# Kernel tuning notes

Hardware: AMD Instinct MI355X
Metric: run time of the kernel (lower is better)

Reference implementation:

```python
import jax, jax.numpy as jnp
import numpy as np

LEAKY_SLOPE = 0.05        # self.alpha is overwritten to 0.05 in __init__
NEG_INF = -9.0e15         # masking constant from the source
THRESH = 0.5              # connection_threshold

B, N, F = 8, 2048, 128


def setup_inputs() -> dict:
    key = jax.random.key(0)
    k1, k2, k3, k4, k5 = jax.random.split(key, 5)
    h = jax.random.normal(k1, (B, N, F), dtype=jnp.float32)
    W = jax.random.normal(k2, (F, F), dtype=jnp.float32) * (1.414 / np.sqrt(F))
    a = jax.random.normal(k3, (2 * F, 1), dtype=jnp.float32) * 0.1
    A1 = jax.random.normal(k4, (4 * N, N), dtype=jnp.float32) * (1.414 / np.sqrt(N))
    A2 = jax.random.normal(k5, (N, 4 * N), dtype=jnp.float32) * (1.414 / np.sqrt(4 * N))
    return {"h": h, "W": W, "a": a, "A1": A1, "A2": A2}


def reference(h, W, a, A1, A2):
    f = W.shape[0]
    # Wh = h @ W^T  (torch Linear stores weight as [out, in])
    Wh = jnp.einsum('bnf,gf->bng', h, W)                       # [B,N,F]
    # additive GAT scores: e[b,i,j] = leaky_relu(Wh_i.a1 + Wh_j.a2)
    Wh1 = Wh @ a[:f, :]                                        # [B,N,1]
    Wh2 = Wh @ a[f:, :]                                        # [B,N,1]
    e = Wh1 + jnp.swapaxes(Wh2, 1, 2)                          # [B,N,N]
    e = jnp.where(e > 0, e, LEAKY_SLOPE * e)                   # LeakyReLU(0.05)
    # learned adjacency gate over last dim (computed in the original forward
    # but never used for the returned output -> dead code; kept for fidelity)
    hid = jax.nn.sigmoid(jnp.einsum('bij,hj->bih', e, A1))     # [B,N,4N]
    adj = jax.nn.sigmoid(e + jnp.einsum('bih,jh->bij', hid, A2))
    adj = jnp.where(adj > THRESH, adj, 0.0)                    # unused downstream
    # masked softmax attention over e itself
    attention = jax.nn.softmax(jnp.where(e > 0, e, NEG_INF), axis=2)
    # dropout is identity in eval mode (training=False)
    h_prime = jnp.einsum('bij,bjf->bif', attention, Wh)        # [B,N,F]
    return jax.nn.elu(h_prime)                                 # concat=True branch
```

## Files before the change

### kernel.cpp

```cpp
#include <hip/hip_runtime.h>
#include <math.h>

#define BB 8
#define NN 2048
#define FF 128
#define CH 128
#define CHSZ 16

__global__ __launch_bounds__(512) void k1_wh(
        const float* __restrict__ h, const float* __restrict__ W,
        const float* __restrict__ a, float* __restrict__ Wh,
        float* __restrict__ s1, float* __restrict__ s2) {
    __shared__ __align__(16) float Wt[64][132];
    __shared__ float hs[64][65];
    const int tid = threadIdx.x;
    const int row0 = blockIdx.x * 64;
    const int gq = tid & 15;
    const int rq = tid >> 4;

    float acc[2][8];
#pragma unroll
    for (int r = 0; r < 2; ++r)
#pragma unroll
        for (int g = 0; g < 8; ++g) acc[r][g] = 0.f;

    for (int half = 0; half < 2; ++half) {
        __syncthreads();
        for (int idx = tid; idx < 64 * 128; idx += 512) {
            int g = idx >> 6, fl = idx & 63;
            Wt[fl][g] = W[g * 128 + half * 64 + fl];
        }
        for (int idx = tid; idx < 64 * 64; idx += 512) {
            int r = idx >> 6, fl = idx & 63;
            hs[r][fl] = h[(row0 + r) * 128 + half * 64 + fl];
        }
        __syncthreads();
        for (int fl = 0; fl < 64; ++fl) {
            float4 w0 = *(const float4*)&Wt[fl][gq * 8];
            float4 w1 = *(const float4*)&Wt[fl][gq * 8 + 4];
            float h0 = hs[rq * 2 + 0][fl];
            float h1 = hs[rq * 2 + 1][fl];
            acc[0][0] += h0 * w0.x; acc[0][1] += h0 * w0.y;
            acc[0][2] += h0 * w0.z; acc[0][3] += h0 * w0.w;
            acc[0][4] += h0 * w1.x; acc[0][5] += h0 * w1.y;
            acc[0][6] += h0 * w1.z; acc[0][7] += h0 * w1.w;
            acc[1][0] += h1 * w0.x; acc[1][1] += h1 * w0.y;
            acc[1][2] += h1 * w0.z; acc[1][3] += h1 * w0.w;
            acc[1][4] += h1 * w1.x; acc[1][5] += h1 * w1.y;
            acc[1][6] += h1 * w1.z; acc[1][7] += h1 * w1.w;
        }
    }

    float a1v[8], a2v[8];
#pragma unroll
    for (int g = 0; g < 8; ++g) {
        a1v[g] = a[gq * 8 + g];
        a2v[g] = a[128 + gq * 8 + g];
    }
#pragma unroll
    for (int r = 0; r < 2; ++r) {
        int row = row0 + rq * 2 + r;
        *(float4*)&Wh[row * 128 + gq * 8] =
            make_float4(acc[r][0], acc[r][1], acc[r][2], acc[r][3]);
        *(float4*)&Wh[row * 128 + gq * 8 + 4] =
            make_float4(acc[r][4], acc[r][5], acc[r][6], acc[r][7]);
        float p1 = 0.f, p2 = 0.f;
#pragma unroll
        for (int g = 0; g < 8; ++g) {
            p1 += acc[r][g] * a1v[g];
            p2 += acc[r][g] * a2v[g];
        }
#pragma unroll
        for (int s = 1; s < 16; s <<= 1) {
            p1 += __shfl_xor(p1, s, 64);
            p2 += __shfl_xor(p2, s, 64);
        }
        if (gq == 0) { s1[row] = p1; s2[row] = p2; }
    }
}

__global__ __launch_bounds__(512) void k2_rank(
        const float* __restrict__ s2, const float* __restrict__ s1,
        int* __restrict__ idxs, float* __restrict__ ps,
        int* __restrict__ lo_arr) {
    __shared__ __align__(16) float ls[NN];
    __shared__ int part[8][64];
    __shared__ int lpart[8][64];
    __shared__ float wmax[8];
    const int t = threadIdx.x;
    const int blk = blockIdx.x;
    const int b = blk >> 5;
    const int seg = blk & 31;
    const int base = b * NN;
    float4* ls4 = (float4*)ls;
    const float4* g4 = (const float4*)(s2 + base);
    float m;
    {
        float4 v4 = g4[t];
        ls4[t] = v4;
        m = fmaxf(fmaxf(v4.x, v4.y), fmaxf(v4.z, v4.w));
    }
#pragma unroll
    for (int s = 1; s < 64; s <<= 1) m = fmaxf(m, __shfl_xor(m, s, 64));
    if ((t & 63) == 0) wmax[t >> 6] = m;
    __syncthreads();
    float M = wmax[0];
#pragma unroll
    for (int i = 1; i < 8; ++i) M = fmaxf(M, wmax[i]);
    const int jj = t & 63;
    const int w  = t >> 6;
    const int j  = seg * 64 + jj;
    const float v = ls[j];
    const float s1v = s1[base + j];
    int rank = 0, cnt = 0;
#pragma unroll 8
    for (int q = 0; q < 64; ++q) {
        float4 kv = ls4[w * 64 + q];
        int kg = w * 256 + q * 4;
        rank += (kv.x < v) | ((kv.x == v) & (kg + 0 < j));
        rank += (kv.y < v) | ((kv.y == v) & (kg + 1 < j));
        rank += (kv.z < v) | ((kv.z == v) & (kg + 2 < j));
        rank += (kv.w < v) | ((kv.w == v) & (kg + 3 < j));
        cnt += (s1v + kv.x <= 0.f);
        cnt += (s1v + kv.y <= 0.f);
        cnt += (s1v + kv.z <= 0.f);
        cnt += (s1v + kv.w <= 0.f);
    }
    part[w][jj] = rank;
    lpart[w][jj] = cnt;
    __syncthreads();
    if (t < 64) {
        int r = 0, lo = 0;
#pragma unroll
        for (int ww = 0; ww < 8; ++ww) {
            r  += part[ww][t];
            lo += lpart[ww][t];
        }
        int jg = seg * 64 + t;
        float vv = ls[jg];
        idxs[base + r] = jg;
        ps[base + r] = expf(vv - M);
        lo_arr[base + jg] = lo;
    }
}

__global__ __launch_bounds__(128) void k3_scan(
        const float* __restrict__ Wh, const int* __restrict__ idxs,
        const float* __restrict__ ps,
        float* __restrict__ partial, float* __restrict__ psuf,
        float* __restrict__ chunktot, float* __restrict__ chunku,
        float* __restrict__ chunkp) {
    const int blk = blockIdx.x;
    const int b = blk >> 7, c = blk & 127;
    const int base = b * NN;
    const int f = threadIdx.x;
    float acc = 0.f, accu = 0.f, pacc = 0.f;
#pragma unroll
    for (int tt = CHSZ - 1; tt >= 0; --tt) {
        int r = c * CHSZ + tt;
        int jj = idxs[base + r];
        float pv = ps[base + r];
        float w = Wh[(base + jj) * 128 + f];
        acc += pv * w;
        accu += w;
        pacc += pv;
        partial[(base + r) * 128 + f] = acc;
        if (f == 0) psuf[base + r] = pacc;
    }
    chunktot[(b * CH + c) * 128 + f] = acc;
    chunku[(b * CH + c) * 128 + f] = accu;
    if (f == 0) chunkp[b * CH + c] = pacc;
}

__global__ __launch_bounds__(512) void k4_merged(
        const float* __restrict__ chunktot, const float* __restrict__ chunku,
        const float* __restrict__ chunkp,
        const int* __restrict__ lo_arr, const float* __restrict__ psuf,
        const float* __restrict__ partial, float* __restrict__ out) {
    __shared__ __align__(16) float cs[CH][132];
    __shared__ __align__(16) float mvp[4][132];
    __shared__ __align__(16) float mv[128];
    __shared__ float lp[CH];
    const int tid = threadIdx.x;
    const int blk = blockIdx.x;
    const int b = blk >> 5;
    const int base = b * NN;

    {
        const int f  = tid & 127;
        const int r0 = tid >> 7;
        float su = 0.f;
#pragma unroll 4
        for (int i = 0; i < 32; ++i) {
            int c = r0 + i * 4;
            cs[c][f] = chunktot[(b * CH + c) * 128 + f];
            su += chunku[(b * CH + c) * 128 + f];
        }
        mvp[r0][f] = su;
        if (tid < CH) lp[tid] = chunkp[b * CH + tid];
    }
    __syncthreads();
    if (tid < 128)
        mv[tid] = (mvp[0][tid] + mvp[1][tid] + mvp[2][tid] + mvp[3][tid])
                  * (1.f / (float)NN);

    for (int s = 1; s < CH; s <<= 1) {
        float tmp[32];
#pragma unroll
        for (int i = 0; i < 32; ++i) {
            int c = (tid >> 7) + i * 4;
            int f = tid & 127;
            tmp[i] = (c + s < CH) ? cs[c + s][f] : 0.f;
        }
        float ap = 0.f;
        if (tid < CH && tid + s < CH) ap = lp[tid + s];
        __syncthreads();
#pragma unroll
        for (int i = 0; i < 32; ++i) {
            int c = (tid >> 7) + i * 4;
            int f = tid & 127;
            cs[c][f] += tmp[i];
        }
        if (tid < CH) lp[tid] += ap;
        __syncthreads();
    }

#pragma unroll
    for (int pass = 0; pass < 4; ++pass) {
        const int rowg = blk * 64 + pass * 16 + (tid >> 5);
        const int fq = (tid & 31) * 4;
        const int lo = lo_arr[rowg];
        float4 v;
        if (lo == NN) {
            v = make_float4(mv[fq], mv[fq + 1], mv[fq + 2], mv[fq + 3]);
        } else {
            const int c = lo >> 4;
            float4 pp = *(const float4*)&partial[(base + lo) * 128 + fq];
            float4 csv = make_float4(0.f, 0.f, 0.f, 0.f);
            float lps = 0.f;
            if (c < CH - 1) {
                csv = *(const float4*)&cs[c + 1][fq];
                lps = lp[c + 1];
            }
            float den = psuf[base + lo] + lps;
            v.x = (pp.x + csv.x) / den;
            v.y = (pp.y + csv.y) / den;
            v.z = (pp.z + csv.z) / den;
            v.w = (pp.w + csv.w) / den;
        }
        v.x = (v.x > 0.f) ? v.x : expm1f(v.x);
        v.y = (v.y > 0.f) ? v.y : expm1f(v.y);
        v.z = (v.z > 0.f) ? v.z : expm1f(v.z);
        v.w = (v.w > 0.f) ? v.w : expm1f(v.w);
        *(float4*)&out[rowg * 128 + fq] = v;
    }
}

extern "C" void kernel_launch(void* const* d_in, const int* in_sizes, int n_in,
                              void* d_out, int out_size, void* d_ws, size_t ws_size,
                              hipStream_t stream) {
    (void)in_sizes; (void)n_in; (void)out_size; (void)ws_size;
    const float* h = (const float*)d_in[0];
    const float* W = (const float*)d_in[1];
    const float* a = (const float*)d_in[2];
    float* out = (float*)d_out;

    float* Wh       = (float*)d_ws;
    float* partial  = Wh + 2097152;
    float* s1       = partial + 2097152;
    float* s2       = s1 + 16384;
    float* ps       = s2 + 16384;
    float* psuf     = ps + 16384;
    int*   idxs     = (int*)(psuf + 16384);
    int*   lo_arr   = idxs + 16384;
    float* chunktot = (float*)(lo_arr + 16384);
    float* chunku   = chunktot + 131072;
    float* chunkp   = chunku + 131072;

    k1_wh<<<BB * NN / 64, 512, 0, stream>>>(h, W, a, Wh, s1, s2);
    k2_rank<<<BB * 32, 512, 0, stream>>>(s2, s1, idxs, ps, lo_arr);
    k3_scan<<<BB * CH, 128, 0, stream>>>(Wh, idxs, ps, partial, psuf,
                                         chunktot, chunku, chunkp);
    k4_merged<<<BB * 32, 512, 0, stream>>>(chunktot, chunku, chunkp,
                                           lo_arr, psuf, partial, out);
}
```

Before: 188.2 us.

## Use split-bf16 MFMA for Wh projection and register-based suffix scan in k4

The Wh = h·W^T projection now runs on MFMA bf16 instructions, with each fp32 operand split into high and low bf16 parts. Three MFMAs per tile (hi·hi, hi·lo, lo·hi) approximate fp32 accuracy. The block drops to 256 threads and W is converted into LDS in both halves per block. Separately, k4 replaces its log-step shared-memory suffix scan over 128 chunks, which needed many syncthreads, with a per-thread serial suffix sum over 32 chunks plus a small cross-segment offset, and does a wavefront-shuffle scan for chunkp. The split-bf16 product drops the lo·lo term, so it risks small precision loss.

New measurement: 170.0 us. -9.6%, faster.

```diff
diff --git a/kernel.cpp b/kernel.cpp
--- a/kernel.cpp
+++ b/kernel.cpp
@@ -7,75 +7,110 @@
 #define CH 128
 #define CHSZ 16
 
-__global__ __launch_bounds__(512) void k1_wh(
+typedef __attribute__((ext_vector_type(8))) short short8;
+typedef __attribute__((ext_vector_type(4))) float f32x4;
+
+__device__ __forceinline__ ushort f2bf(float x) {
+    uint u = __float_as_uint(x);
+    uint r = (u + 0x7FFFu + ((u >> 16) & 1u)) >> 16;
+    return (ushort)r;
+}
+__device__ __forceinline__ float bf2f(ushort x) {
+    return __uint_as_float(((uint)x) << 16);
+}
+
+__global__ __launch_bounds__(256) void k1_wh(
         const float* __restrict__ h, const float* __restrict__ W,
         const float* __restrict__ a, float* __restrict__ Wh,
         float* __restrict__ s1, float* __restrict__ s2) {
-    __shared__ __align__(16) float Wt[64][132];
-    __shared__ float hs[64][65];
+    __shared__ __align__(16) ushort Whi[128][136];
+    __shared__ __align__(16) ushort Wlo[128][136];
+    __shared__ __align__(16) ushort hhi[64][136];
+    __shared__ __align__(16) ushort hlo[64][136];
     const int tid = threadIdx.x;
     const int row0 = blockIdx.x * 64;
-    const int gq = tid & 15;
-    const int rq = tid >> 4;
-
-    float acc[2][8];
-#pragma unroll
-    for (int r = 0; r < 2; ++r)
-#pragma unroll
-        for (int g = 0; g < 8; ++g) acc[r][g] = 0.f;
-
-    for (int half = 0; half < 2; ++half) {
-        __syncthreads();
-        for (int idx = tid; idx < 64 * 128; idx += 512) {
-            int g = idx >> 6, fl = idx & 63;
-            Wt[fl][g] = W[g * 128 + half * 64 + fl];
-        }
-        for (int idx = tid; idx < 64 * 64; idx += 512) {
-            int r = idx >> 6, fl = idx & 63;
-            hs[r][fl] = h[(row0 + r) * 128 + half * 64 + fl];
-        }
-        __syncthreads();
-        for (int fl = 0; fl < 64; ++fl) {
-            float4 w0 = *(const float4*)&Wt[fl][gq * 8];
-            float4 w1 = *(const float4*)&Wt[fl][gq * 8 + 4];
-            float h0 = hs[rq * 2 + 0][fl];
-            float h1 = hs[rq * 2 + 1][fl];
-            acc[0][0] += h0 * w0.x; acc[0][1] += h0 * w0.y;
-            acc[0][2] += h0 * w0.z; acc[0][3] += h0 * w0.w;
-            acc[0][4] += h0 * w1.x; acc[0][5] += h0 * w1.y;
-            acc[0][6] += h0 * w1.z; acc[0][7] += h0 * w1.w;
-            acc[1][0] += h1 * w0.x; acc[1][1] += h1 * w0.y;
-            acc[1][2] += h1 * w0.z; acc[1][3] += h1 * w0.w;
-            acc[1][4] += h1 * w1.x; acc[1][5] += h1 * w1.y;
-            acc[1][6] += h1 * w1.z; acc[1][7] += h1 * w1.w;
-        }
-    }
-
-    float a1v[8], a2v[8];
-#pragma unroll
-    for (int g = 0; g < 8; ++g) {
-        a1v[g] = a[gq * 8 + g];
-        a2v[g] = a[128 + gq * 8 + g];
-    }
-#pragma unroll
-    for (int r = 0; r < 2; ++r) {
-        int row = row0 + rq * 2 + r;
-        *(float4*)&Wh[row * 128 + gq * 8] =
-            make_float4(acc[r][0], acc[r][1], acc[r][2], acc[r][3]);
-        *(float4*)&Wh[row * 128 + gq * 8 + 4] =
-            make_float4(acc[r][4], acc[r][5], acc[r][6], acc[r][7]);
-        float p1 = 0.f, p2 = 0.f;
-#pragma unroll
-        for (int g = 0; g < 8; ++g) {
-            p1 += acc[r][g] * a1v[g];
-            p2 += acc[r][g] * a2v[g];
-        }
-#pragma unroll
-        for (int s = 1; s < 16; s <<= 1) {
-            p1 += __shfl_xor(p1, s, 64);
-            p2 += __shfl_xor(p2, s, 64);
-        }
-        if (gq == 0) { s1[row] = p1; s2[row] = p2; }
+
+    for (int i = tid; i < 4096; i += 256) {
+        int g = i >> 5, k4 = (i & 31) * 4;
+        float4 wv = *(const float4*)&W[g * 128 + k4];
+        ushort h0 = f2bf(wv.x), h1 = f2bf(wv.y), h2 = f2bf(wv.z), h3 = f2bf(wv.w);
+        ushort l0 = f2bf(wv.x - bf2f(h0)), l1 = f2bf(wv.y - bf2f(h1));
+        ushort l2 = f2bf(wv.z - bf2f(h2)), l3 = f2bf(wv.w - bf2f(h3));
+        uint2 hw, lw;
+        hw.x = (uint)h0 | ((uint)h1 << 16); hw.y = (uint)h2 | ((uint)h3 << 16);
+        lw.x = (uint)l0 | ((uint)l1 << 16); lw.y = (uint)l2 | ((uint)l3 << 16);
+        *(uint2*)&Whi[g][k4] = hw;
+        *(uint2*)&Wlo[g][k4] = lw;
+    }
+    for (int i = tid; i < 2048; i += 256) {
+        int r = i >> 5, k4 = (i & 31) * 4;
+        float4 hv = *(const float4*)&h[(row0 + r) * 128 + k4];
+        ushort h0 = f2bf(hv.x), h1 = f2bf(hv.y), h2 = f2bf(hv.z), h3 = f2bf(hv.w);
+        ushort l0 = f2bf(hv.x - bf2f(h0)), l1 = f2bf(hv.y - bf2f(h1));
+        ushort l2 = f2bf(hv.z - bf2f(h2)), l3 = f2bf(hv.w - bf2f(h3));
+        uint2 hw, lw;
+        hw.x = (uint)h0 | ((uint)h1 << 16); hw.y = (uint)h2 | ((uint)h3 << 16);
+        lw.x = (uint)l0 | ((uint)l1 << 16); lw.y = (uint)l2 | ((uint)l3 << 16);
+        *(uint2*)&hhi[r][k4] = hw;
+        *(uint2*)&hlo[r][k4] = lw;
+    }
+    __syncthreads();
+
+    const int lane = tid & 63;
+    const int wid = tid >> 6;
+    const int gl = lane & 15;
+    const int kg = lane >> 4;
+    const int lr = wid * 16 + gl;
+
+    f32x4 acc[8];
+#pragma unroll
+    for (int gt = 0; gt < 8; ++gt) acc[gt] = (f32x4){0.f, 0.f, 0.f, 0.f};
+
+#pragma unroll
+    for (int t = 0; t < 4; ++t) {
+        const int k0 = t * 32 + kg * 8;
+        short8 ah = *(const short8*)&hhi[lr][k0];
+        short8 al = *(const short8*)&hlo[lr][k0];
+#pragma unroll
+        for (int gt = 0; gt < 8; ++gt) {
+            const int g = gt * 16 + gl;
+            short8 bh = *(const short8*)&Whi[g][k0];
+            short8 bl = *(const short8*)&Wlo[g][k0];
+            acc[gt] = __builtin_amdgcn_mfma_f32_16x16x32_bf16(ah, bh, acc[gt], 0, 0, 0);
+            acc[gt] = __builtin_amdgcn_mfma_f32_16x16x32_bf16(ah, bl, acc[gt], 0, 0, 0);
+            acc[gt] = __builtin_amdgcn_mfma_f32_16x16x32_bf16(al, bh, acc[gt], 0, 0, 0);
+        }
+    }
+
+    float p1a[4] = {0.f, 0.f, 0.f, 0.f}, p2a[4] = {0.f, 0.f, 0.f, 0.f};
+#pragma unroll
+    for (int gt = 0; gt < 8; ++gt) {
+        const int g = gt * 16 + gl;
+        const float a1v = a[g];
+        const float a2v = a[128 + g];
+#pragma unroll
+        for (int r = 0; r < 4; ++r) {
+            float wvv = acc[gt][r];
+            Wh[(row0 + wid * 16 + kg * 4 + r) * 128 + g] = wvv;
+            p1a[r] += wvv * a1v;
+            p2a[r] += wvv * a2v;
+        }
+    }
+#pragma unroll
+    for (int s = 1; s < 16; s <<= 1) {
+#pragma unroll
+        for (int r = 0; r < 4; ++r) {
+            p1a[r] += __shfl_xor(p1a[r], s, 64);
+            p2a[r] += __shfl_xor(p2a[r], s, 64);
+        }
+    }
+    if (gl == 0) {
+#pragma unroll
+        for (int r = 0; r < 4; ++r) {
+            int row = row0 + wid * 16 + kg * 4 + r;
+            s1[row] = p1a[r];
+            s2[row] = p2a[r];
+        }
     }
 }
 
@@ -178,52 +213,57 @@
         const int* __restrict__ lo_arr, const float* __restrict__ psuf,
         const float* __restrict__ partial, float* __restrict__ out) {
     __shared__ __align__(16) float cs[CH][132];
-    __shared__ __align__(16) float mvp[4][132];
-    __shared__ __align__(16) float mv[128];
+    __shared__ float segt[4][128];
+    __shared__ float mvp[4][128];
+    __shared__ float mv[128];
     __shared__ float lp[CH];
     const int tid = threadIdx.x;
     const int blk = blockIdx.x;
     const int b = blk >> 5;
     const int base = b * NN;
-
-    {
-        const int f  = tid & 127;
-        const int r0 = tid >> 7;
-        float su = 0.f;
-#pragma unroll 4
-        for (int i = 0; i < 32; ++i) {
-            int c = r0 + i * 4;
-            cs[c][f] = chunktot[(b * CH + c) * 128 + f];
-            su += chunku[(b * CH + c) * 128 + f];
-        }
-        mvp[r0][f] = su;
-        if (tid < CH) lp[tid] = chunkp[b * CH + tid];
-    }
-    __syncthreads();
+    const int f = tid & 127;
+    const int q = tid >> 7;
+
+    float suf[32];
+    float acc = 0.f, su = 0.f;
+#pragma unroll
+    for (int i = 31; i >= 0; --i) {
+        int c = q * 32 + i;
+        acc += chunktot[(b * CH + c) * 128 + f];
+        su  += chunku[(b * CH + c) * 128 + f];
+        suf[i] = acc;
+    }
+    segt[q][f] = acc;
+    mvp[q][f] = su;
+
+    if (tid < 64) {
+        float p0 = chunkp[b * CH + tid * 2];
+        float p1v = chunkp[b * CH + tid * 2 + 1];
+        float S = p0 + p1v;
+        float T = S;
+#pragma unroll
+        for (int s = 1; s < 64; s <<= 1) {
+            float t2 = __shfl_down(T, s, 64);
+            if (tid + s < 64) T += t2;
+        }
+        float E = __shfl_down(T, 1, 64);
+        if (tid == 63) E = 0.f;
+        lp[tid * 2]     = p0 + p1v + E;
+        lp[tid * 2 + 1] = p1v + E;
+    }
+    __syncthreads();
+
+    float off = 0.f;
+#pragma unroll
+    for (int qq = 1; qq < 4; ++qq)
+        if (q + qq < 4) off += segt[q + qq][f];
+#pragma unroll
+    for (int i = 0; i < 32; ++i)
+        cs[q * 32 + i][f] = suf[i] + off;
     if (tid < 128)
         mv[tid] = (mvp[0][tid] + mvp[1][tid] + mvp[2][tid] + mvp[3][tid])
                   * (1.f / (float)NN);
-
-    for (int s = 1; s < CH; s <<= 1) {
-        float tmp[32];
-#pragma unroll
-        for (int i = 0; i < 32; ++i) {
-            int c = (tid >> 7) + i * 4;
-            int f = tid & 127;
-            tmp[i] = (c + s < CH) ? cs[c + s][f] : 0.f;
-        }
-        float ap = 0.f;
-        if (tid < CH && tid + s < CH) ap = lp[tid + s];
-        __syncthreads();
-#pragma unroll
-        for (int i = 0; i < 32; ++i) {
-            int c = (tid >> 7) + i * 4;
-            int f = tid & 127;
-            cs[c][f] += tmp[i];
-        }
-        if (tid < CH) lp[tid] += ap;
-        __syncthreads();
-    }
+    __syncthreads();
 
 #pragma unroll
     for (int pass = 0; pass < 4; ++pass) {
@@ -277,7 +317,7 @@
     float* chunku   = chunktot + 131072;
     float* chunkp   = chunku + 131072;
 
-    k1_wh<<<BB * NN / 64, 512, 0, stream>>>(h, W, a, Wh, s1, s2);
+    k1_wh<<<BB * NN / 64, 256, 0, stream>>>(h, W, a, Wh, s1, s2);
     k2_rank<<<BB * 32, 512, 0, stream>>>(s2, s1, idxs, ps, lo_arr);
     k3_scan<<<BB * CH, 128, 0, stream>>>(Wh, idxs, ps, partial, psuf,
                                          chunktot, chunku, chunkp);
```
